# Performance work log

Hardware: AMD Instinct MI355X
Metric: run time of the kernel (lower is better)

Reference implementation:

```python
import jax, jax.numpy as jnp
import numpy as np

N_NODES = 100000
N_FEAT = 256
OUT_DIM = 128
NNZ_X = 1_600_000
NNZ_A = 1_600_000
DROPOUT = 0.0  # layer default; floor(1-p+u) mask is all-ones -> deterministic


def setup_inputs() -> dict:
    key = jax.random.key(0)
    k = jax.random.split(key, 7)
    feat_rows = jax.random.randint(k[0], (NNZ_X,), 0, N_NODES, dtype=jnp.int32)
    feat_cols = jax.random.randint(k[1], (NNZ_X,), 0, N_FEAT, dtype=jnp.int32)
    feat_vals = jax.random.normal(k[2], (NNZ_X,), dtype=jnp.float32)
    adj_rows = jax.random.randint(k[3], (NNZ_A,), 0, N_NODES, dtype=jnp.int32)
    adj_cols = jax.random.randint(k[4], (NNZ_A,), 0, N_NODES, dtype=jnp.int32)
    adj_vals = jax.random.uniform(k[5], (NNZ_A,), dtype=jnp.float32)
    glorot_std = np.sqrt(2.0 / (N_FEAT + OUT_DIM)).astype(np.float32)
    W = jax.random.normal(k[6], (N_FEAT, OUT_DIM), dtype=jnp.float32) * glorot_std
    return {
        "feat_rows": feat_rows, "feat_cols": feat_cols, "feat_vals": feat_vals,
        "adj_rows": adj_rows, "adj_cols": adj_cols, "adj_vals": adj_vals,
        "W": W, "n_nodes": N_NODES,
    }


def reference(feat_rows, feat_cols, feat_vals, adj_rows, adj_cols, adj_vals, W, n_nodes):
    # sparse dropout on feature nonzeros: mask = floor((1-p) + uniform) in {0,1}
    u = jax.random.uniform(jax.random.key(1), feat_vals.shape, dtype=feat_vals.dtype)
    keep = jnp.floor((1.0 - DROPOUT) + u)
    vals = feat_vals * keep * (1.0 / (1.0 - DROPOUT))
    # X @ W : gather W rows by feature column, scale by nnz value, scatter-add into node rows
    xw = jax.ops.segment_sum(vals[:, None] * W[feat_cols], feat_rows,
                             num_segments=n_nodes)  # [N, D]
    # A @ (X @ W) : gather node rows by edge source, scale by edge weight, scatter-add to dest
    agg = jax.ops.segment_sum(adj_vals[:, None] * xw[adj_cols], adj_rows,
                              num_segments=n_nodes)  # [N, D]
    return jax.nn.relu(agg)
```

## Files before the change

kernel.cpp:

```cpp
#include <hip/hip_runtime.h>
#include <hip/hip_fp16.h>

#define OUT_DIM 128
#define NPS 256
#define NS_MAX 400
#define CAP_S 4608
#define CURSTR 32
#define SBLK1 1024
#define EPT1 4
#define CHUNK1 (SBLK1 * EPT1)
#define SBLK2 1024
#define EPT2 5
#define GBLK 256

__device__ __forceinline__ void scatter1_body(
    const int* __restrict__ rows, const int* __restrict__ cols,
    const float* __restrict__ vals, int nnz, int chunk,
    int* __restrict__ cur, int2* __restrict__ pay, int ns, int matbase)
{
    __shared__ int2 s_stage[CHUNK1];
    __shared__ unsigned short s_bin[CHUNK1];
    __shared__ int s_hist[NS_MAX];
    __shared__ int s_excl[NS_MAX];
    __shared__ int s_gbase[NS_MAX];

    int tid = threadIdx.x;
    int start = chunk * CHUNK1;
    int total = nnz - start; if (total > CHUNK1) total = CHUNK1;

    for (int i = tid; i < ns; i += SBLK1) s_hist[i] = 0;
    __syncthreads();

    int rr[EPT1]; int cc[EPT1]; float vv[EPT1];
    #pragma unroll
    for (int k = 0; k < EPT1; ++k) {
        int e = start + k * SBLK1 + tid;
        rr[k] = -1;
        if (e < nnz) {
            rr[k] = rows[e]; cc[k] = cols[e]; vv[k] = vals[e];
            atomicAdd(&s_hist[rr[k] >> 8], 1);
        }
    }
    __syncthreads();

    if (tid < 64) {
        int carry = 0;
        for (int seg = 0; seg < ns; seg += 64) {
            int idx = seg + tid;
            int x = (idx < ns) ? s_hist[idx] : 0;
            int incl = x;
            #pragma unroll
            for (int off = 1; off < 64; off <<= 1) {
                int y = __shfl_up(incl, off, 64);
                if (tid >= off) incl += y;
            }
            if (idx < ns) s_excl[idx] = carry + incl - x;
            carry += __shfl(incl, 63, 64);
        }
    }
    __syncthreads();

    for (int i = tid; i < ns; i += SBLK1) {
        int c = s_hist[i];
        s_gbase[i] = (c > 0) ? atomicAdd(&cur[(matbase + i) * CURSTR], c) : 0;
        s_hist[i] = 0;
    }
    __syncthreads();

    #pragma unroll
    for (int k = 0; k < EPT1; ++k) {
        if (rr[k] >= 0) {
            int b = rr[k] >> 8;
            int rl = rr[k] & 255;
            int pos = s_excl[b] + atomicAdd(&s_hist[b], 1);
            s_stage[pos] = make_int2((rl << 17) | cc[k], __float_as_int(vv[k]));
            s_bin[pos] = (unsigned short)b;
        }
    }
    __syncthreads();

    for (int i = tid; i < total; i += SBLK1) {
        int b = s_bin[i];
        int g = s_gbase[b] + (i - s_excl[b]);
        if (g < CAP_S)
            pay[(size_t)(matbase + b) * CAP_S + g] = s_stage[i];
    }
}

__global__ __launch_bounds__(SBLK1) void scatter1x_kernel(
    const int* __restrict__ rows, const int* __restrict__ cols,
    const float* __restrict__ vals, int nnz,
    int* __restrict__ cur, int2* __restrict__ pay, int ns)
{
    scatter1_body(rows, cols, vals, nnz, blockIdx.x, cur, pay, ns, ns);
}

__device__ __forceinline__ void sort2_body(
    const int* __restrict__ cur, int2* __restrict__ pay,
    int2* __restrict__ row_span, int b, int ns, int n_nodes)
{
    __shared__ int s_cnt[NPS];
    __shared__ int s_excl2[NPS];
    int tid = threadIdx.x;
    int count = cur[b * CURSTR]; if (count > CAP_S) count = CAP_S;
    int2* region = pay + (size_t)b * CAP_S;

    if (tid < NPS) s_cnt[tid] = 0;
    __syncthreads();

    int2 er[EPT2];
    #pragma unroll
    for (int k = 0; k < EPT2; ++k) {
        int i = tid + k * SBLK2;
        er[k] = make_int2(-1, 0);
        if (i < count) {
            er[k] = region[i];
            atomicAdd(&s_cnt[((unsigned)er[k].x) >> 17], 1);
        }
    }
    __syncthreads();

    if (tid < 64) {
        int carry = 0;
        #pragma unroll
        for (int seg = 0; seg < NPS; seg += 64) {
            int x = s_cnt[seg + tid];
            int incl = x;
            #pragma unroll
            for (int off = 1; off < 64; off <<= 1) {
                int y = __shfl_up(incl, off, 64);
                if (tid >= off) incl += y;
            }
            s_excl2[seg + tid] = carry + incl - x;
            carry += __shfl(incl, 63, 64);
        }
    }
    __syncthreads();

    int m = (b >= ns) ? 1 : 0;
    if (tid < NPS) {
        int g = (b - m * ns) * NPS + tid;
        if (g < n_nodes)
            row_span[(size_t)m * n_nodes + g] =
                make_int2(b * CAP_S + s_excl2[tid], s_cnt[tid]);
    }
    __syncthreads();

    #pragma unroll
    for (int k = 0; k < EPT2; ++k) {
        if (er[k].x >= 0) {
            int rl = ((unsigned)er[k].x) >> 17;
            int pos = atomicAdd(&s_excl2[rl], 1);
            region[pos] = make_int2(er[k].x & 0x1FFFF, er[k].y);
        }
    }
}

__global__ __launch_bounds__(SBLK1) void scA_s2x_kernel(
    const int* __restrict__ adj_rows, const int* __restrict__ adj_cols,
    const float* __restrict__ adj_vals, int nnz_a, int nCkA,
    int* __restrict__ cur, int2* __restrict__ pay,
    int2* __restrict__ row_span, int ns, int n_nodes)
{
    if ((int)blockIdx.x < nCkA) {
        scatter1_body(adj_rows, adj_cols, adj_vals, nnz_a, blockIdx.x,
                      cur, pay, ns, 0);
    } else {
        sort2_body(cur, pay, row_span, ns + ((int)blockIdx.x - nCkA), ns, n_nodes);
    }
}

__global__ void wcast_kernel(const float* __restrict__ W, __half* __restrict__ W16, int n) {
    int i = blockIdx.x * blockDim.x + threadIdx.x;
    if (i < n) W16[i] = __float2half(W[i]);
}

__global__ __launch_bounds__(SBLK2) void sortA_xw_kernel(
    const int* __restrict__ cur, int2* __restrict__ pay,
    int2* __restrict__ row_span,
    const __half* __restrict__ W16, __half* __restrict__ XW,
    int ns, int n_nodes)
{
    if ((int)blockIdx.x < ns) {
        sort2_body(cur, pay, row_span, blockIdx.x, ns, n_nodes);
        return;
    }
    int tid = threadIdx.x;
    int lane = tid & 15;
    int node = ((int)blockIdx.x - ns) * 64 + (tid >> 4);
    if (node >= n_nodes) return;
    int2 span = row_span[(size_t)n_nodes + node];
    int s = span.x, cnt = span.y;
    const int4* Wv = (const int4*)W16;
    float a0=0,a1=0,a2=0,a3=0,a4=0,a5=0,a6=0,a7=0;
    for (int base = 0; base < cnt; base += 16) {
        int mm = cnt - base; if (mm > 16) mm = 16;
        int2 pl = make_int2(0, 0);
        if (lane < mm) pl = pay[s + base + lane];
        #pragma unroll 4
        for (int j = 0; j < mm; ++j) {
            int c = __shfl(pl.x, j, 16);
            float v = __int_as_float(__shfl(pl.y, j, 16));
            union { int4 i4; __half2 h[4]; } u;
            u.i4 = Wv[(size_t)c * 16 + lane];
            float2 f0 = __half22float2(u.h[0]);
            float2 f1 = __half22float2(u.h[1]);
            float2 f2 = __half22float2(u.h[2]);
            float2 f3 = __half22float2(u.h[3]);
            a0 += v * f0.x; a1 += v * f0.y; a2 += v * f1.x; a3 += v * f1.y;
            a4 += v * f2.x; a5 += v * f2.y; a6 += v * f3.x; a7 += v * f3.y;
        }
    }
    union { int4 i4; __half2 h[4]; } o;
    o.h[0] = __floats2half2_rn(a0, a1);
    o.h[1] = __floats2half2_rn(a2, a3);
    o.h[2] = __floats2half2_rn(a4, a5);
    o.h[3] = __floats2half2_rn(a6, a7);
    ((int4*)(XW + (size_t)node * OUT_DIM))[lane] = o.i4;
}

__global__ __launch_bounds__(GBLK, 4) void gather_agg_kernel(
    const int2* __restrict__ row_span, const int2* __restrict__ pay,
    const __half* __restrict__ XW, float* __restrict__ out, int n_nodes)
{
    int tid = threadIdx.x;
    int lane = tid & 15;
    int node = blockIdx.x * 16 + (tid >> 4);
    if (node >= n_nodes) return;
    int2 span = row_span[node];
    int s = span.x, cnt = span.y;
    const int4* Xv = (const int4*)XW;
    float a0=0,a1=0,a2=0,a3=0,a4=0,a5=0,a6=0,a7=0;
    int2 pl = make_int2(0, 0);
    if (lane < cnt) pl = pay[s + lane];
    for (int base = 0; base < cnt; base += 16) {
        int4 w[16];
        #pragma unroll
        for (int j = 0; j < 16; ++j) {
            int c = __shfl(pl.x, j, 16);
            w[j] = Xv[(size_t)((c << 4) | lane)];
        }
        int2 pln = make_int2(0, 0);
        if (base + 16 + lane < cnt) pln = pay[s + base + 16 + lane];
        #pragma unroll
        for (int j = 0; j < 16; ++j) {
            float v = __int_as_float(__shfl(pl.y, j, 16));
            union { int4 i4; __half2 h[4]; } u;
            u.i4 = w[j];
            float2 f0 = __half22float2(u.h[0]);
            float2 f1 = __half22float2(u.h[1]);
            float2 f2 = __half22float2(u.h[2]);
            float2 f3 = __half22float2(u.h[3]);
            a0 += v * f0.x; a1 += v * f0.y; a2 += v * f1.x; a3 += v * f1.y;
            a4 += v * f2.x; a5 += v * f2.y; a6 += v * f3.x; a7 += v * f3.y;
        }
        pl = pln;
    }
    float4 lo, hi;
    lo.x = fmaxf(a0, 0.f); lo.y = fmaxf(a1, 0.f);
    lo.z = fmaxf(a2, 0.f); lo.w = fmaxf(a3, 0.f);
    hi.x = fmaxf(a4, 0.f); hi.y = fmaxf(a5, 0.f);
    hi.z = fmaxf(a6, 0.f); hi.w = fmaxf(a7, 0.f);
    float4* orow = (float4*)(out + (size_t)node * OUT_DIM);
    orow[2 * lane]     = lo;
    orow[2 * lane + 1] = hi;
}

extern "C" void kernel_launch(void* const* d_in, const int* in_sizes, int n_in,
                              void* d_out, int out_size, void* d_ws, size_t ws_size,
                              hipStream_t stream) {
    const int*   feat_rows = (const int*)d_in[0];
    const int*   feat_cols = (const int*)d_in[1];
    const float* feat_vals = (const float*)d_in[2];
    const int*   adj_rows  = (const int*)d_in[3];
    const int*   adj_cols  = (const int*)d_in[4];
    const float* adj_vals  = (const float*)d_in[5];
    const float* W         = (const float*)d_in[6];
    float*       out       = (float*)d_out;

    const int nnz_x   = in_sizes[0];
    const int nnz_a   = in_sizes[3];
    const int n_w     = in_sizes[6];
    const int n_nodes = out_size / OUT_DIM;
    const int ns      = (n_nodes + NPS - 1) / NPS;

    char* p = (char*)d_ws;
    __half* XW   = (__half*)p;  p += (size_t)n_nodes * OUT_DIM * sizeof(__half);
    __half* W16  = (__half*)p;  p += (size_t)n_w * sizeof(__half);
    p = (char*)(((uintptr_t)p + 127) & ~(uintptr_t)127);
    int2* pay    = (int2*)p;    p += (size_t)2 * ns * CAP_S * sizeof(int2);
    int2* row_span = (int2*)p;  p += (size_t)2 * n_nodes * sizeof(int2);
    p = (char*)(((uintptr_t)p + 127) & ~(uintptr_t)127);
    int* cur     = (int*)p;     p += (size_t)2 * ns * CURSTR * sizeof(int);

    (void)hipMemsetAsync(cur, 0, (size_t)2 * ns * CURSTR * sizeof(int), stream);

    wcast_kernel<<<(n_w + 255) / 256, 256, 0, stream>>>(W, W16, n_w);

    const int nCkA = (nnz_a + CHUNK1 - 1) / CHUNK1;
    const int nCkX = (nnz_x + CHUNK1 - 1) / CHUNK1;

    scatter1x_kernel<<<nCkX, SBLK1, 0, stream>>>(
        feat_rows, feat_cols, feat_vals, nnz_x, cur, pay, ns);

    scA_s2x_kernel<<<nCkA + ns, SBLK1, 0, stream>>>(
        adj_rows, adj_cols, adj_vals, nnz_a, nCkA,
        cur, pay, row_span, ns, n_nodes);

    const int gnb64 = (n_nodes + 63) / 64;
    sortA_xw_kernel<<<ns + gnb64, SBLK2, 0, stream>>>(
        cur, pay, row_span, W16, XW, ns, n_nodes);

    const int gnb = (n_nodes + 15) / 16;
    gather_agg_kernel<<<gnb, GBLK, 0, stream>>>(row_span, pay, XW, out, n_nodes);
}
```

Before: 235.2 us.

## Fuse per-bucket row sort into gather kernels using LDS, shrink buckets to 64 rows

Buckets shrink from 256 to 64 rows, so a bucket's edges (up to 1280) fit in shared memory. The second-pass counting sort now runs in LDS inside the gather kernels rather than in separate sort passes that rewrote the payload and wrote a row_span array. This removes two global read/write passes over the sorted payload and one launch. The costs are a fourfold larger bin count in the first scatter, with more global atomics and smaller write runs, and lower per-block parallelism in the gathers (1024-thread blocks with 64 nodes). Rows beyond the tighter capacity are dropped silently.

```diff
diff --git a/kernel.cpp b/kernel.cpp
--- a/kernel.cpp
+++ b/kernel.cpp
@@ -2,33 +2,31 @@
 #include <hip/hip_fp16.h>
 
 #define OUT_DIM 128
-#define NPS 256
-#define NS_MAX 400
-#define CAP_S 4608
+#define NPB 64
+#define NB_MAX 1600
+#define CAP_B 1280
 #define CURSTR 32
 #define SBLK1 1024
 #define EPT1 4
 #define CHUNK1 (SBLK1 * EPT1)
-#define SBLK2 1024
-#define EPT2 5
-#define GBLK 256
+#define FBLK 1024
 
 __device__ __forceinline__ void scatter1_body(
     const int* __restrict__ rows, const int* __restrict__ cols,
     const float* __restrict__ vals, int nnz, int chunk,
-    int* __restrict__ cur, int2* __restrict__ pay, int ns, int matbase)
+    int* __restrict__ cur, int2* __restrict__ pay, int nb, int matbase)
 {
     __shared__ int2 s_stage[CHUNK1];
     __shared__ unsigned short s_bin[CHUNK1];
-    __shared__ int s_hist[NS_MAX];
-    __shared__ int s_excl[NS_MAX];
-    __shared__ int s_gbase[NS_MAX];
+    __shared__ int s_hist[NB_MAX];
+    __shared__ int s_excl[NB_MAX];
+    __shared__ int s_gbase[NB_MAX];
 
     int tid = threadIdx.x;
     int start = chunk * CHUNK1;
     int total = nnz - start; if (total > CHUNK1) total = CHUNK1;
 
-    for (int i = tid; i < ns; i += SBLK1) s_hist[i] = 0;
+    for (int i = tid; i < nb; i += SBLK1) s_hist[i] = 0;
     __syncthreads();
 
     int rr[EPT1]; int cc[EPT1]; float vv[EPT1];
@@ -38,29 +36,29 @@
         rr[k] = -1;
         if (e < nnz) {
             rr[k] = rows[e]; cc[k] = cols[e]; vv[k] = vals[e];
-            atomicAdd(&s_hist[rr[k] >> 8], 1);
+            atomicAdd(&s_hist[rr[k] >> 6], 1);
         }
     }
     __syncthreads();
 
     if (tid < 64) {
         int carry = 0;
-        for (int seg = 0; seg < ns; seg += 64) {
+        for (int seg = 0; seg < nb; seg += 64) {
             int idx = seg + tid;
-            int x = (idx < ns) ? s_hist[idx] : 0;
+            int x = (idx < nb) ? s_hist[idx] : 0;
             int incl = x;
             #pragma unroll
             for (int off = 1; off < 64; off <<= 1) {
                 int y = __shfl_up(incl, off, 64);
                 if (tid >= off) incl += y;
             }
-            if (idx < ns) s_excl[idx] = carry + incl - x;
+            if (idx < nb) s_excl[idx] = carry + incl - x;
             carry += __shfl(incl, 63, 64);
         }
     }
     __syncthreads();
 
-    for (int i = tid; i < ns; i += SBLK1) {
+    for (int i = tid; i < nb; i += SBLK1) {
         int c = s_hist[i];
         s_gbase[i] = (c > 0) ? atomicAdd(&cur[(matbase + i) * CURSTR], c) : 0;
         s_hist[i] = 0;
@@ -70,8 +68,8 @@
     #pragma unroll
     for (int k = 0; k < EPT1; ++k) {
         if (rr[k] >= 0) {
-            int b = rr[k] >> 8;
-            int rl = rr[k] & 255;
+            int b = rr[k] >> 6;
+            int rl = rr[k] & 63;
             int pos = s_excl[b] + atomicAdd(&s_hist[b], 1);
             s_stage[pos] = make_int2((rl << 17) | cc[k], __float_as_int(vv[k]));
             s_bin[pos] = (unsigned short)b;
@@ -82,92 +80,17 @@
     for (int i = tid; i < total; i += SBLK1) {
         int b = s_bin[i];
         int g = s_gbase[b] + (i - s_excl[b]);
-        if (g < CAP_S)
-            pay[(size_t)(matbase + b) * CAP_S + g] = s_stage[i];
+        if (g < CAP_B)
+            pay[(size_t)(matbase + b) * CAP_B + g] = s_stage[i];
     }
 }
 
 __global__ __launch_bounds__(SBLK1) void scatter1x_kernel(
     const int* __restrict__ rows, const int* __restrict__ cols,
     const float* __restrict__ vals, int nnz,
-    int* __restrict__ cur, int2* __restrict__ pay, int ns)
-{
-    scatter1_body(rows, cols, vals, nnz, blockIdx.x, cur, pay, ns, ns);
-}
-
-__device__ __forceinline__ void sort2_body(
-    const int* __restrict__ cur, int2* __restrict__ pay,
-    int2* __restrict__ row_span, int b, int ns, int n_nodes)
-{
-    __shared__ int s_cnt[NPS];
-    __shared__ int s_excl2[NPS];
-    int tid = threadIdx.x;
-    int count = cur[b * CURSTR]; if (count > CAP_S) count = CAP_S;
-    int2* region = pay + (size_t)b * CAP_S;
-
-    if (tid < NPS) s_cnt[tid] = 0;
-    __syncthreads();
-
-    int2 er[EPT2];
-    #pragma unroll
-    for (int k = 0; k < EPT2; ++k) {
-        int i = tid + k * SBLK2;
-        er[k] = make_int2(-1, 0);
-        if (i < count) {
-            er[k] = region[i];
-            atomicAdd(&s_cnt[((unsigned)er[k].x) >> 17], 1);
-        }
-    }
-    __syncthreads();
-
-    if (tid < 64) {
-        int carry = 0;
-        #pragma unroll
-        for (int seg = 0; seg < NPS; seg += 64) {
-            int x = s_cnt[seg + tid];
-            int incl = x;
-            #pragma unroll
-            for (int off = 1; off < 64; off <<= 1) {
-                int y = __shfl_up(incl, off, 64);
-                if (tid >= off) incl += y;
-            }
-            s_excl2[seg + tid] = carry + incl - x;
-            carry += __shfl(incl, 63, 64);
-        }
-    }
-    __syncthreads();
-
-    int m = (b >= ns) ? 1 : 0;
-    if (tid < NPS) {
-        int g = (b - m * ns) * NPS + tid;
-        if (g < n_nodes)
-            row_span[(size_t)m * n_nodes + g] =
-                make_int2(b * CAP_S + s_excl2[tid], s_cnt[tid]);
-    }
-    __syncthreads();
-
-    #pragma unroll
-    for (int k = 0; k < EPT2; ++k) {
-        if (er[k].x >= 0) {
-            int rl = ((unsigned)er[k].x) >> 17;
-            int pos = atomicAdd(&s_excl2[rl], 1);
-            region[pos] = make_int2(er[k].x & 0x1FFFF, er[k].y);
-        }
-    }
-}
-
-__global__ __launch_bounds__(SBLK1) void scA_s2x_kernel(
-    const int* __restrict__ adj_rows, const int* __restrict__ adj_cols,
-    const float* __restrict__ adj_vals, int nnz_a, int nCkA,
-    int* __restrict__ cur, int2* __restrict__ pay,
-    int2* __restrict__ row_span, int ns, int n_nodes)
-{
-    if ((int)blockIdx.x < nCkA) {
-        scatter1_body(adj_rows, adj_cols, adj_vals, nnz_a, blockIdx.x,
-                      cur, pay, ns, 0);
-    } else {
-        sort2_body(cur, pay, row_span, ns + ((int)blockIdx.x - nCkA), ns, n_nodes);
-    }
+    int* __restrict__ cur, int2* __restrict__ pay, int nb)
+{
+    scatter1_body(rows, cols, vals, nnz, blockIdx.x, cur, pay, nb, nb);
 }
 
 __global__ void wcast_kernel(const float* __restrict__ W, __half* __restrict__ W16, int n) {
@@ -175,73 +98,76 @@
     if (i < n) W16[i] = __float2half(W[i]);
 }
 
-__global__ __launch_bounds__(SBLK2) void sortA_xw_kernel(
-    const int* __restrict__ cur, int2* __restrict__ pay,
-    int2* __restrict__ row_span,
-    const __half* __restrict__ W16, __half* __restrict__ XW,
-    int ns, int n_nodes)
-{
-    if ((int)blockIdx.x < ns) {
-        sort2_body(cur, pay, row_span, blockIdx.x, ns, n_nodes);
-        return;
-    }
+template <bool IS_XW>
+__device__ __forceinline__ void fused_gather_body(
+    const int* __restrict__ cur, const int2* __restrict__ pay,
+    const __half* __restrict__ table,
+    __half* __restrict__ XW, float* __restrict__ out,
+    int b, int nb, int n_nodes)
+{
+    __shared__ int2 s_edge[CAP_B];
+    __shared__ int s_cnt[NPB];
+    __shared__ int s_excl[NPB];
     int tid = threadIdx.x;
+    int matbase = IS_XW ? nb : 0;
+    int count = cur[(matbase + b) * CURSTR]; if (count > CAP_B) count = CAP_B;
+    const int2* region = pay + (size_t)(matbase + b) * CAP_B;
+
+    if (tid < NPB) s_cnt[tid] = 0;
+    __syncthreads();
+
+    int2 e0 = make_int2(-1, 0), e1 = make_int2(-1, 0);
+    if (tid < count) {
+        e0 = region[tid];
+        atomicAdd(&s_cnt[((unsigned)e0.x) >> 17], 1);
+    }
+    if (tid + FBLK < count) {
+        e1 = region[tid + FBLK];
+        atomicAdd(&s_cnt[((unsigned)e1.x) >> 17], 1);
+    }
+    __syncthreads();
+
+    if (tid < 64) {
+        int x = s_cnt[tid];
+        int incl = x;
+        #pragma unroll
+        for (int off = 1; off < 64; off <<= 1) {
+            int y = __shfl_up(incl, off, 64);
+            if (tid >= off) incl += y;
+        }
+        s_excl[tid] = incl - x;
+    }
+    __syncthreads();
+
+    if (e0.x >= 0) {
+        int rl = ((unsigned)e0.x) >> 17;
+        int pos = atomicAdd(&s_excl[rl], 1);
+        if (pos < CAP_B) s_edge[pos] = e0;
+    }
+    if (e1.x >= 0) {
+        int rl = ((unsigned)e1.x) >> 17;
+        int pos = atomicAdd(&s_excl[rl], 1);
+        if (pos < CAP_B) s_edge[pos] = e1;
+    }
+    __syncthreads();
+
     int lane = tid & 15;
-    int node = ((int)blockIdx.x - ns) * 64 + (tid >> 4);
+    int grp = tid >> 4;
+    int node = b * NPB + grp;
     if (node >= n_nodes) return;
-    int2 span = row_span[(size_t)n_nodes + node];
-    int s = span.x, cnt = span.y;
-    const int4* Wv = (const int4*)W16;
+    int cnt = s_cnt[grp];
+    int gstart = s_excl[grp] - cnt;
+    const int4* Tv = (const int4*)table;
     float a0=0,a1=0,a2=0,a3=0,a4=0,a5=0,a6=0,a7=0;
     for (int base = 0; base < cnt; base += 16) {
-        int mm = cnt - base; if (mm > 16) mm = 16;
         int2 pl = make_int2(0, 0);
-        if (lane < mm) pl = pay[s + base + lane];
-        #pragma unroll 4
-        for (int j = 0; j < mm; ++j) {
-            int c = __shfl(pl.x, j, 16);
-            float v = __int_as_float(__shfl(pl.y, j, 16));
-            union { int4 i4; __half2 h[4]; } u;
-            u.i4 = Wv[(size_t)c * 16 + lane];
-            float2 f0 = __half22float2(u.h[0]);
-            float2 f1 = __half22float2(u.h[1]);
-            float2 f2 = __half22float2(u.h[2]);
-            float2 f3 = __half22float2(u.h[3]);
-            a0 += v * f0.x; a1 += v * f0.y; a2 += v * f1.x; a3 += v * f1.y;
-            a4 += v * f2.x; a5 += v * f2.y; a6 += v * f3.x; a7 += v * f3.y;
-        }
-    }
-    union { int4 i4; __half2 h[4]; } o;
-    o.h[0] = __floats2half2_rn(a0, a1);
-    o.h[1] = __floats2half2_rn(a2, a3);
-    o.h[2] = __floats2half2_rn(a4, a5);
-    o.h[3] = __floats2half2_rn(a6, a7);
-    ((int4*)(XW + (size_t)node * OUT_DIM))[lane] = o.i4;
-}
-
-__global__ __launch_bounds__(GBLK, 4) void gather_agg_kernel(
-    const int2* __restrict__ row_span, const int2* __restrict__ pay,
-    const __half* __restrict__ XW, float* __restrict__ out, int n_nodes)
-{
-    int tid = threadIdx.x;
-    int lane = tid & 15;
-    int node = blockIdx.x * 16 + (tid >> 4);
-    if (node >= n_nodes) return;
-    int2 span = row_span[node];
-    int s = span.x, cnt = span.y;
-    const int4* Xv = (const int4*)XW;
-    float a0=0,a1=0,a2=0,a3=0,a4=0,a5=0,a6=0,a7=0;
-    int2 pl = make_int2(0, 0);
-    if (lane < cnt) pl = pay[s + lane];
-    for (int base = 0; base < cnt; base += 16) {
+        if (base + lane < cnt) pl = s_edge[gstart + base + lane];
         int4 w[16];
         #pragma unroll
         for (int j = 0; j < 16; ++j) {
-            int c = __shfl(pl.x, j, 16);
-            w[j] = Xv[(size_t)((c << 4) | lane)];
-        }
-        int2 pln = make_int2(0, 0);
-        if (base + 16 + lane < cnt) pln = pay[s + base + 16 + lane];
+            int c = __shfl(pl.x, j, 16) & 0x1FFFF;
+            w[j] = Tv[(size_t)((c << 4) | lane)];
+        }
         #pragma unroll
         for (int j = 0; j < 16; ++j) {
             float v = __int_as_float(__shfl(pl.y, j, 16));
@@ -254,16 +180,49 @@
             a0 += v * f0.x; a1 += v * f0.y; a2 += v * f1.x; a3 += v * f1.y;
             a4 += v * f2.x; a5 += v * f2.y; a6 += v * f3.x; a7 += v * f3.y;
         }
-        pl = pln;
-    }
-    float4 lo, hi;
-    lo.x = fmaxf(a0, 0.f); lo.y = fmaxf(a1, 0.f);
-    lo.z = fmaxf(a2, 0.f); lo.w = fmaxf(a3, 0.f);
-    hi.x = fmaxf(a4, 0.f); hi.y = fmaxf(a5, 0.f);
-    hi.z = fmaxf(a6, 0.f); hi.w = fmaxf(a7, 0.f);
-    float4* orow = (float4*)(out + (size_t)node * OUT_DIM);
-    orow[2 * lane]     = lo;
-    orow[2 * lane + 1] = hi;
+    }
+    if (IS_XW) {
+        union { int4 i4; __half2 h[4]; } o;
+        o.h[0] = __floats2half2_rn(a0, a1);
+        o.h[1] = __floats2half2_rn(a2, a3);
+        o.h[2] = __floats2half2_rn(a4, a5);
+        o.h[3] = __floats2half2_rn(a6, a7);
+        ((int4*)(XW + (size_t)node * OUT_DIM))[lane] = o.i4;
+    } else {
+        float4 lo, hi;
+        lo.x = fmaxf(a0, 0.f); lo.y = fmaxf(a1, 0.f);
+        lo.z = fmaxf(a2, 0.f); lo.w = fmaxf(a3, 0.f);
+        hi.x = fmaxf(a4, 0.f); hi.y = fmaxf(a5, 0.f);
+        hi.z = fmaxf(a6, 0.f); hi.w = fmaxf(a7, 0.f);
+        float4* orow = (float4*)(out + (size_t)node * OUT_DIM);
+        orow[2 * lane]     = lo;
+        orow[2 * lane + 1] = hi;
+    }
+}
+
+__global__ __launch_bounds__(SBLK1) void scA_fxw_kernel(
+    const int* __restrict__ adj_rows, const int* __restrict__ adj_cols,
+    const float* __restrict__ adj_vals, int nnz_a, int nCkA,
+    int* __restrict__ cur, int2* __restrict__ pay,
+    const __half* __restrict__ W16, __half* __restrict__ XW,
+    int nb, int n_nodes)
+{
+    if ((int)blockIdx.x < nCkA) {
+        scatter1_body(adj_rows, adj_cols, adj_vals, nnz_a, blockIdx.x,
+                      cur, pay, nb, 0);
+    } else {
+        fused_gather_body<true>(cur, pay, W16, XW, nullptr,
+                                (int)blockIdx.x - nCkA, nb, n_nodes);
+    }
+}
+
+__global__ __launch_bounds__(FBLK) void fused_agg_kernel(
+    const int* __restrict__ cur, const int2* __restrict__ pay,
+    const __half* __restrict__ XW, float* __restrict__ out,
+    int nb, int n_nodes)
+{
+    fused_gather_body<false>(cur, pay, XW, nullptr, out,
+                             blockIdx.x, nb, n_nodes);
 }
 
 extern "C" void kernel_launch(void* const* d_in, const int* in_sizes, int n_in,
@@ -282,18 +241,17 @@
     const int nnz_a   = in_sizes[3];
     const int n_w     = in_sizes[6];
     const int n_nodes = out_size / OUT_DIM;
-    const int ns      = (n_nodes + NPS - 1) / NPS;
+    const int nb      = (n_nodes + NPB - 1) / NPB;
 
     char* p = (char*)d_ws;
     __half* XW   = (__half*)p;  p += (size_t)n_nodes * OUT_DIM * sizeof(__half);
     __half* W16  = (__half*)p;  p += (size_t)n_w * sizeof(__half);
     p = (char*)(((uintptr_t)p + 127) & ~(uintptr_t)127);
-    int2* pay    = (int2*)p;    p += (size_t)2 * ns * CAP_S * sizeof(int2);
-    int2* row_span = (int2*)p;  p += (size_t)2 * n_nodes * sizeof(int2);
+    int2* pay    = (int2*)p;    p += (size_t)2 * nb * CAP_B * sizeof(int2);
     p = (char*)(((uintptr_t)p + 127) & ~(uintptr_t)127);
-    int* cur     = (int*)p;     p += (size_t)2 * ns * CURSTR * sizeof(int);
-
-    (void)hipMemsetAsync(cur, 0, (size_t)2 * ns * CURSTR * sizeof(int), stream);
+    int* cur     = (int*)p;     p += (size_t)2 * nb * CURSTR * sizeof(int);
+
+    (void)hipMemsetAsync(cur, 0, (size_t)2 * nb * CURSTR * sizeof(int), stream);
 
     wcast_kernel<<<(n_w + 255) / 256, 256, 0, stream>>>(W, W16, n_w);
 
@@ -301,16 +259,11 @@
     const int nCkX = (nnz_x + CHUNK1 - 1) / CHUNK1;
 
     scatter1x_kernel<<<nCkX, SBLK1, 0, stream>>>(
-        feat_rows, feat_cols, feat_vals, nnz_x, cur, pay, ns);
-
-    scA_s2x_kernel<<<nCkA + ns, SBLK1, 0, stream>>>(
+        feat_rows, feat_cols, feat_vals, nnz_x, cur, pay, nb);
+
+    scA_fxw_kernel<<<nCkA + nb, SBLK1, 0, stream>>>(
         adj_rows, adj_cols, adj_vals, nnz_a, nCkA,
-        cur, pay, row_span, ns, n_nodes);
-
-    const int gnb64 = (n_nodes + 63) / 64;
-    sortA_xw_kernel<<<ns + gnb64, SBLK2, 0, stream>>>(
-        cur, pay, row_span, W16, XW, ns, n_nodes);
-
-    const int gnb = (n_nodes + 15) / 16;
-    gather_agg_kernel<<<gnb, GBLK, 0, stream>>>(row_span, pay, XW, out, n_nodes);
-}
+        cur, pay, W16, XW, nb, n_nodes);
+
+    fused_agg_kernel<<<nb, FBLK, 0, stream>>>(cur, pay, XW, out, nb, n_nodes);
+}
```

Result: slower. 280.8 us (+19.4%).
